# Optimization experiments

Hardware: AMD Instinct MI355X
Metric: run time of the kernel (lower is better)

The kernel has to match this reference:

```python
import jax, jax.numpy as jnp
import numpy as np

N_TOK = 256
C_Z = 128
C = 32
N_HEAD = 4


def setup_inputs() -> dict:
    key = jax.random.key(0)
    ks = jax.random.split(key, 8)
    s = 0.02
    return {
        "z": jax.random.normal(ks[0], (N_TOK, N_TOK, C_Z), dtype=jnp.float32),
        "single_mask": jnp.ones((N_TOK,), dtype=jnp.float32),
        "ln_gamma": jnp.ones((C_Z,), dtype=jnp.float32),
        "ln_beta": jnp.zeros((C_Z,), dtype=jnp.float32),
        "W_q": jax.random.normal(ks[1], (C_Z, N_HEAD * C), dtype=jnp.float32) * s,
        "W_k": jax.random.normal(ks[2], (C_Z, N_HEAD * C), dtype=jnp.float32) * s,
        "W_v": jax.random.normal(ks[3], (C_Z, N_HEAD * C), dtype=jnp.float32) * s,
        "W_b": jax.random.normal(ks[4], (C_Z, N_HEAD), dtype=jnp.float32) * s,
        "W_g": jax.random.normal(ks[5], (C_Z, N_HEAD * C), dtype=jnp.float32) * s,
        "W_out": jax.random.normal(ks[6], (N_HEAD * C, C_Z), dtype=jnp.float32) * s,
    }


def reference(z, single_mask, ln_gamma, ln_beta, W_q, W_k, W_v, W_b, W_g, W_out):
    # LayerNorm over c_z
    mu = jnp.mean(z, axis=-1, keepdims=True)
    var = jnp.var(z, axis=-1, keepdims=True)
    zn = (z - mu) * jax.lax.rsqrt(var + 1e-5) * ln_gamma + ln_beta

    n = zn.shape[0]
    proj = lambda W: (zn @ W).reshape(n, n, N_HEAD, C)
    q = proj(W_q)
    k = proj(W_k)
    v = proj(W_v)
    g = proj(W_g)
    b = zn @ W_b  # [i, j, h] -> used as bias b[j, k, h]

    # a[i,j,k,h] = q[i,j]·k[i,k]/sqrt(c) + b[j,k,h]
    a = jnp.einsum('ijhc,ikhc->ijkh', q, k) / np.sqrt(C).astype(np.float32)
    a = a + b[None, :, :, :]
    a = a + (-1e9) * (1.0 - single_mask)[None, None, :, None]
    a = jax.nn.softmax(a, axis=-2)  # over k

    o = jnp.einsum('ijkh,ikhc->ijhc', a, v)
    o = jax.nn.sigmoid(g) * o
    o = o.reshape(n, n, N_HEAD * C)
    return o @ W_out
```

## Files before the change

kernel.cpp:

```cpp
#include <hip/hip_runtime.h>
#include <hip/hip_bf16.h>

#define NT 256
#define CZ 128
#define CH 32
#define NH 4
#define PL 2097152

typedef unsigned short ushort_t;
typedef unsigned int uint_t;
typedef __attribute__((ext_vector_type(8))) short short8;
typedef __attribute__((ext_vector_type(4))) float f32x4;

__device__ __forceinline__ float bfbits2f(uint_t bits){
  union { uint_t u; float f; } v; v.u = bits; return v.f;
}
__device__ __forceinline__ float bf2f(ushort_t u){
  return bfbits2f(((uint_t)u) << 16);
}
__device__ __forceinline__ ushort_t f2bf(float f){
  union { float f; uint_t u; } v; v.f = f;
  uint_t u = v.u;
  uint_t r = (u + 0x7fffu + ((u >> 16) & 1u)) >> 16;
  return (ushort_t)r;
}
__device__ __forceinline__ void unpk(uint_t w, float& lo, float& hi){
  lo = bfbits2f(w << 16);
  hi = bfbits2f(w & 0xffff0000u);
}
__device__ __forceinline__ short8 as_s8(uint4 u){
  union { uint4 u; short8 s; } v; v.u = u; return v.s;
}
__device__ __forceinline__ uint_t pk2(float a, float b){
  union { __hip_bfloat16 h; ushort_t u; } x, y;
  x.h = __float2bfloat16(a); y.h = __float2bfloat16(b);
  return (uint_t)x.u | ((uint_t)y.u << 16);
}
__device__ __forceinline__ int detect_f32(const ushort_t* zz){
  int l = threadIdx.x & 63;
  int bad = 0;
  #pragma unroll
  for(int s=0;s<4;s++){
    float v = bf2f(zz[l*4 + s]);
    if(!(fabsf(v) < 1e9f)) bad = 1;
  }
  return (__ballot(bad) != 0ull) ? 1 : 0;
}

__global__ __launch_bounds__(256) void k_cvt_wt(const void* __restrict__ s0,
    const void* __restrict__ s1, const void* __restrict__ s2,
    const void* __restrict__ s3, const void* __restrict__ s4,
    ushort_t* __restrict__ dst, const ushort_t* __restrict__ zz,
    const void* __restrict__ m_, const void* __restrict__ g_,
    const void* __restrict__ b_, const void* __restrict__ wb_,
    float* __restrict__ smallf){
  int isf32 = detect_f32(zz);
  if(blockIdx.x >= 320){
    int idx = threadIdx.x * 4;
    const void* sp; int off;
    if(idx < 256){ sp = m_;  off = idx; }
    else if(idx < 384){ sp = g_;  off = idx-256; }
    else if(idx < 512){ sp = b_;  off = idx-384; }
    else { sp = wb_; off = idx-512; }
    float4 o;
    if(isf32){ o = *(const float4*)((const float*)sp + off); }
    else {
      uint2 u = *(const uint2*)((const ushort_t*)sp + off);
      unpk(u.x, o.x, o.y); unpk(u.y, o.z, o.w);
    }
    *(float4*)(smallf + idx) = o;
    return;
  }
  const void* srcs[5] = {s0,s1,s2,s3,s4};
  int w = blockIdx.x >> 6;
  int idx = (blockIdx.x & 63)*256 + threadIdx.x;
  int k = idx >> 7, c = idx & 127;
  const void* sp = srcs[w];
  float v;
  if(isf32) v = ((const float*)sp)[idx];
  else      v = bf2f(((const ushort_t*)sp)[idx]);
  dst[(size_t)w*16384 + (size_t)c*128 + k] = f2bf(v);
}

__global__ __launch_bounds__(256) void k_lnproj(const void* __restrict__ zraw,
    const float* __restrict__ smallf, const ushort_t* __restrict__ Wt,
    ushort_t* __restrict__ qh, ushort_t* __restrict__ kh,
    ushort_t* __restrict__ vh, ushort_t* __restrict__ gh,
    float* __restrict__ btm){
  __shared__ __align__(16) char lds[37888];
  ushort_t* znl = (ushort_t*)lds;
  float*    wbs = (float*)(lds + 35840);
  const float* mkf = smallf;
  const float* gmf = smallf + 256;
  const float* btf = smallf + 384;
  const float* Wbf = smallf + 512;
  int t = threadIdx.x;
  int isf32 = detect_f32((const ushort_t*)zraw);
  wbs[t] = Wbf[t]; wbs[t+256] = Wbf[t+256];
  __syncthreads();

  int row_loc = t >> 1, half = t & 1;
  size_t r = (size_t)blockIdx.x*128 + row_loc;
  float mval = -1e9f * (1.f - mkf[r & 255]);
  float s = 0.f, s2 = 0.f;
  if(isf32){
    const float4* zp = (const float4*)((const float*)zraw + r*CZ + half*64);
    #pragma unroll
    for(int q=0;q<16;q++){
      float4 v = zp[q];
      s  += (v.x + v.y) + (v.z + v.w);
      s2 += (v.x*v.x + v.y*v.y) + (v.z*v.z + v.w*v.w);
    }
  } else {
    const uint4* zp = (const uint4*)((const ushort_t*)zraw + r*CZ + half*64);
    #pragma unroll
    for(int q=0;q<8;q++){
      uint4 u = zp[q];
      const uint_t* pu = (const uint_t*)&u;
      #pragma unroll
      for(int e=0;e<4;e++){
        float lo, hi; unpk(pu[e], lo, hi);
        s += lo + hi; s2 += lo*lo + hi*hi;
      }
    }
  }
  s  += __shfl_xor(s, 1);
  s2 += __shfl_xor(s2, 1);
  float mu  = s * (1.f/CZ);
  float var = fmaxf(s2 * (1.f/CZ) - mu*mu, 0.f);
  float rs  = rsqrtf(var + 1e-5f);
  float acch[4] = {0.f,0.f,0.f,0.f};
  #pragma unroll
  for(int chunk=0;chunk<8;chunk++){
    float v8[8];
    if(isf32){
      const float4* zp = (const float4*)((const float*)zraw + r*CZ + half*64 + chunk*8);
      float4 a = zp[0], b = zp[1];
      v8[0]=a.x; v8[1]=a.y; v8[2]=a.z; v8[3]=a.w;
      v8[4]=b.x; v8[5]=b.y; v8[6]=b.z; v8[7]=b.w;
    } else {
      uint4 u = *(const uint4*)((const ushort_t*)zraw + r*CZ + half*64 + chunk*8);
      const uint_t* pu = (const uint_t*)&u;
      #pragma unroll
      for(int e=0;e<4;e++) unpk(pu[e], v8[e*2], v8[e*2+1]);
    }
    uint_t ow[4];
    #pragma unroll
    for(int e2=0;e2<4;e2++){
      int cg = half*64 + chunk*8 + e2*2;
      float v0 = (v8[e2*2]   - mu)*rs*gmf[cg]   + btf[cg];
      float v1 = (v8[e2*2+1] - mu)*rs*gmf[cg+1] + btf[cg+1];
      float4 w0 = *(const float4*)&wbs[cg*4];
      float4 w1 = *(const float4*)&wbs[(cg+1)*4];
      acch[0] += v0*w0.x + v1*w1.x;
      acch[1] += v0*w0.y + v1*w1.y;
      acch[2] += v0*w0.z + v1*w1.z;
      acch[3] += v0*w0.w + v1*w1.w;
      ow[e2] = (uint_t)f2bf(v0) | ((uint_t)f2bf(v1) << 16);
    }
    uint4 o; o.x=ow[0]; o.y=ow[1]; o.z=ow[2]; o.w=ow[3];
    *(uint4*)(znl + row_loc*140 + half*64 + chunk*8) = o;
  }
  #pragma unroll
  for(int h=0;h<4;h++){
    float tot = acch[h] + __shfl_xor(acch[h], 1);
    if(half == 0) btm[(size_t)h*65536 + r] = (tot + mval) * 1.4426950408889634f;
  }
  __syncthreads();

  int wave = t>>6, l = t&63, n = l&15, quad = l>>4;
  uint4 af[2][4];
  #pragma unroll
  for(int mt=0;mt<2;mt++)
    #pragma unroll
    for(int kb=0;kb<4;kb++)
      af[mt][kb] = *(const uint4*)(znl + (wave*32 + mt*16 + n)*140 + kb*32 + quad*8);
  ushort_t* outs[4] = {qh, kh, vh, gh};
  size_t row0 = (size_t)blockIdx.x*128 + wave*32;
  #pragma unroll
  for(int w=0;w<4;w++){
    const ushort_t* W = Wt + (size_t)w*16384;
    ushort_t* D = outs[w];
    float sc = (w==0) ? (0.17677669529663687f * 1.4426950408889634f) : 1.f;
    #pragma unroll
    for(int nt=0;nt<8;nt++){
      uint4 bfr[4];
      #pragma unroll
      for(int kb=0;kb<4;kb++)
        bfr[kb] = *(const uint4*)(W + ((size_t)(nt*16 + n))*128 + kb*32 + quad*8);
      f32x4 a0 = {0.f,0.f,0.f,0.f}, a1 = {0.f,0.f,0.f,0.f};
      #pragma unroll
      for(int kb=0;kb<4;kb++){
        a0 = __builtin_amdgcn_mfma_f32_16x16x32_bf16(as_s8(bfr[kb]), as_s8(af[0][kb]), a0, 0,0,0);
        a1 = __builtin_amdgcn_mfma_f32_16x16x32_bf16(as_s8(bfr[kb]), as_s8(af[1][kb]), a1, 0,0,0);
      }
      uint2 s0p, s1p;
      s0p.x = pk2(a0[0]*sc, a0[1]*sc); s0p.y = pk2(a0[2]*sc, a0[3]*sc);
      s1p.x = pk2(a1[0]*sc, a1[1]*sc); s1p.y = pk2(a1[2]*sc, a1[3]*sc);
      ushort_t* Db = D + (size_t)(nt>>1)*PL + (size_t)(nt&1)*16 + quad*4;
      *(uint2*)(Db + (row0 + n)*CH)      = s0p;
      *(uint2*)(Db + (row0 + 16 + n)*CH) = s1p;
    }
  }
}

__global__ __launch_bounds__(256, 2) void k_attn(
    const ushort_t* __restrict__ qh, const ushort_t* __restrict__ kh,
    const ushort_t* __restrict__ vh, const ushort_t* __restrict__ gh,
    const float* __restrict__ btm, ushort_t* __restrict__ oh){
  __shared__ __align__(16) char lds[40960];
  uint4*    VfA = (uint4*)lds;
  uint4*    Kf  = (uint4*)(lds + 16384);
  ushort_t* Pw0 = (ushort_t*)(lds + 32768);
  int t = threadIdx.x;
  int i = blockIdx.x >> 2, h = blockIdx.x & 3;
  int wave = t >> 6, l = t & 63;
  int n = l & 15, quad = l >> 4;
  const ushort_t* qhp = qh + (size_t)h*PL + (size_t)(i*NT)*CH;
  const ushort_t* khp = kh + (size_t)h*PL + (size_t)(i*NT)*CH;
  const ushort_t* vhp = vh + (size_t)h*PL + (size_t)(i*NT)*CH;
  const ushort_t* ghp = gh + (size_t)h*PL + (size_t)(i*NT)*CH;
  ushort_t*       ohp = oh + (size_t)h*PL + (size_t)(i*NT)*CH;
  const float*    bth = btm + (size_t)h*65536;

  {
    #pragma unroll
    for(int m=0;m<4;m++){
      int kt = wave*4 + m;
      Kf[kt*64 + l] = *(const uint4*)(khp + (size_t)(kt*16 + n)*CH + quad*8);
    }
  }
  {
    #pragma unroll
    for(int it=0; it<4; it++){
      int u = wave + it*4, kblk = u >> 1, ct = u & 1;
      uint_t d[4];
      #pragma unroll
      for(int e=0;e<4;e++){
        uint_t lo = vhp[(size_t)(kblk*32 + quad*8 + e*2    )*CH + ct*16 + n];
        uint_t hi = vhp[(size_t)(kblk*32 + quad*8 + e*2 + 1)*CH + ct*16 + n];
        d[e] = lo | (hi << 16);
      }
      uint4 o; o.x=d[0]; o.y=d[1]; o.z=d[2]; o.w=d[3];
      VfA[u*64 + l] = o;
    }
  }
  __syncthreads();

  ushort_t* Pw = Pw0 + wave*1024;
  int swz = (n & 7) << 4;

  #pragma unroll 1
  for(int s=0;s<4;s++){
    int jt = wave*4 + s;
    uint4 qf = *(const uint4*)(qhp + (size_t)(jt*16 + n)*CH + quad*8);
    f32x4 acc[16];
    #pragma unroll
    for(int kt=0;kt<16;kt++)
      acc[kt] = *(const f32x4*)(bth + (size_t)(jt*16 + n)*256 + kt*16 + quad*4);
    #pragma unroll
    for(int kt=0;kt<16;kt++){
      uint4 kfv = Kf[kt*64 + l];
      acc[kt] = __builtin_amdgcn_mfma_f32_16x16x32_bf16(as_s8(kfv), as_s8(qf), acc[kt], 0,0,0);
    }
    float sum0 = 0.f, sum1 = 0.f;
    f32x4 oa0 = {0.f,0.f,0.f,0.f}, oa1 = {0.f,0.f,0.f,0.f};
    #pragma unroll
    for(int H=0;H<2;H++){
      uint2 pv[8];
      #pragma unroll
      for(int kt=0;kt<8;kt++){
        float e0 = __builtin_amdgcn_exp2f(acc[H*8+kt][0]);
        float e1 = __builtin_amdgcn_exp2f(acc[H*8+kt][1]);
        float e2 = __builtin_amdgcn_exp2f(acc[H*8+kt][2]);
        float e3 = __builtin_amdgcn_exp2f(acc[H*8+kt][3]);
        sum0 += e0 + e1; sum1 += e2 + e3;
        pv[kt].x = pk2(e0, e1);
        pv[kt].y = pk2(e2, e3);
      }
      #pragma unroll
      for(int Q2=0;Q2<2;Q2++){
        #pragma unroll
        for(int m=0;m<4;m++)
          *(uint2*)((char*)Pw + (((n<<7) + (m<<5) + (quad<<3)) ^ swz)) = pv[Q2*4+m];
        #pragma unroll
        for(int kb=0;kb<2;kb++){
          uint4 pf = *(const uint4*)((char*)Pw + (((n<<7) + (kb<<6) + (quad<<4)) ^ swz));
          int kg = (H*2+Q2)*2 + kb;
          oa0 = __builtin_amdgcn_mfma_f32_16x16x32_bf16(as_s8(VfA[(kg*2+0)*64 + l]), as_s8(pf), oa0, 0,0,0);
          oa1 = __builtin_amdgcn_mfma_f32_16x16x32_bf16(as_s8(VfA[(kg*2+1)*64 + l]), as_s8(pf), oa1, 0,0,0);
        }
      }
    }
    float ssum = sum0 + sum1;
    ssum += __shfl_xor(ssum, 16);
    ssum += __shfl_xor(ssum, 32);
    float inv = 1.f / ssum;
    size_t rb = (size_t)(jt*16 + n)*CH;
    uint2 g0 = *(const uint2*)(ghp + rb + quad*4);
    uint2 g1 = *(const uint2*)(ghp + rb + 16 + quad*4);
    float ga[4], gc[4];
    unpk(g0.x, ga[0], ga[1]); unpk(g0.y, ga[2], ga[3]);
    unpk(g1.x, gc[0], gc[1]); unpk(g1.y, gc[2], gc[3]);
    float v0[4], v1[4];
    #pragma unroll
    for(int rr=0;rr<4;rr++){
      v0[rr] = oa0[rr] * inv * (1.f/(1.f + __expf(-ga[rr])));
      v1[rr] = oa1[rr] * inv * (1.f/(1.f + __expf(-gc[rr])));
    }
    uint2 s0, s1;
    s0.x = (uint_t)f2bf(v0[0]) | ((uint_t)f2bf(v0[1]) << 16);
    s0.y = (uint_t)f2bf(v0[2]) | ((uint_t)f2bf(v0[3]) << 16);
    s1.x = (uint_t)f2bf(v1[0]) | ((uint_t)f2bf(v1[1]) << 16);
    s1.y = (uint_t)f2bf(v1[2]) | ((uint_t)f2bf(v1[3]) << 16);
    *(uint2*)(ohp + rb + quad*4)      = s0;
    *(uint2*)(ohp + rb + 16 + quad*4) = s1;
  }
}

__global__ __launch_bounds__(256) void k_gemm1(const ushort_t* __restrict__ oh,
    const ushort_t* __restrict__ Wt, void* __restrict__ outp,
    const ushort_t* __restrict__ zz){
  int isf32 = detect_f32(zz);
  int t = threadIdx.x, wave = t>>6, l = t&63, n = l&15, quad = l>>4;
  size_t row0 = (size_t)blockIdx.x*128 + wave*32;
  uint4 af[2][4];
  #pragma unroll
  for(int mt=0;mt<2;mt++)
    #pragma unroll
    for(int kb=0;kb<4;kb++)
      af[mt][kb] = *(const uint4*)(oh + (size_t)kb*PL + (row0 + mt*16 + n)*CH + quad*8);
  #pragma unroll
  for(int nt=0;nt<8;nt++){
    uint4 bfr[4];
    #pragma unroll
    for(int kb=0;kb<4;kb++)
      bfr[kb] = *(const uint4*)(Wt + ((size_t)(nt*16 + n))*128 + kb*32 + quad*8);
    f32x4 a0 = {0.f,0.f,0.f,0.f}, a1 = {0.f,0.f,0.f,0.f};
    #pragma unroll
    for(int kb=0;kb<4;kb++){
      a0 = __builtin_amdgcn_mfma_f32_16x16x32_bf16(as_s8(bfr[kb]), as_s8(af[0][kb]), a0, 0,0,0);
      a1 = __builtin_amdgcn_mfma_f32_16x16x32_bf16(as_s8(bfr[kb]), as_s8(af[1][kb]), a1, 0,0,0);
    }
    if(isf32){
      float* of = (float*)outp + nt*16 + quad*4;
      *(f32x4*)(of + (row0 + n)*CZ)      = a0;
      *(f32x4*)(of + (row0 + 16 + n)*CZ) = a1;
    } else {
      uint2 s0p, s1p;
      s0p.x = pk2(a0[0], a0[1]); s0p.y = pk2(a0[2], a0[3]);
      s1p.x = pk2(a1[0], a1[1]); s1p.y = pk2(a1[2], a1[3]);
      ushort_t* ob = (ushort_t*)outp + nt*16 + quad*4;
      *(uint2*)(ob + (row0 + n)*CZ)      = s0p;
      *(uint2*)(ob + (row0 + 16 + n)*CZ) = s1p;
    }
  }
}

extern "C" void kernel_launch(void* const* d_in, const int* in_sizes, int n_in,
                              void* d_out, int out_size, void* d_ws, size_t ws_size,
                              hipStream_t stream){
  char* wsb = (char*)d_ws;
  const size_t TB = (size_t)16777216;
  ushort_t* qh  = (ushort_t*)(wsb);
  ushort_t* kh  = (ushort_t*)(wsb + TB);
  ushort_t* vh  = (ushort_t*)(wsb + 2*TB);
  ushort_t* gh  = (ushort_t*)(wsb + 3*TB);
  ushort_t* oh  = (ushort_t*)(wsb + 4*TB);
  float*    btm = (float*)   (wsb + 5*TB);
  float*  smallf= (float*)   (wsb + 5*TB + (1u<<20));
  ushort_t* Wt  = (ushort_t*)(wsb + 5*TB + (1u<<20) + 4096);
  const ushort_t* zz = (const ushort_t*)d_in[0];

  k_cvt_wt   <<<321, 256, 0, stream>>>(d_in[4], d_in[5], d_in[6], d_in[8], d_in[9],
                                       Wt, zz, d_in[1], d_in[2], d_in[3], d_in[7], smallf);
  k_lnproj   <<<512, 256, 0, stream>>>(d_in[0], smallf, Wt, qh, kh, vh, gh, btm);
  k_attn     <<<1024,256, 0, stream>>>(qh, kh, vh, gh, btm, oh);
  k_gemm1    <<<512, 256, 0, stream>>>(oh, Wt + (size_t)4*16384, d_out, zz);
}
```

Measured before the change: 209.7 us.

## Fuse output projection GEMM into attention kernel with one block per row

The attention kernel is restructured so each 512-thread block handles one row i for all four heads, with two waves per head sharing that head's K and V tiles in a larger LDS allocation. After a barrier, the same block runs the final W_out projection over the 256 gated outputs it just wrote, which removes the separate k_gemm1 launch and lets those reads likely hit cache. The trade-off is a grid of only 256 blocks and about 144 KB of LDS per block, which limits each CU to one resident block and may hurt latency hiding. Each wave also now works through twice as many j-tiles in sequence.

Result: faster. 197.5 us, median of 2 (-5.8%).

```diff
diff --git a/kernel.cpp b/kernel.cpp
--- a/kernel.cpp
+++ b/kernel.cpp
@@ -204,18 +204,21 @@
   }
 }
 
-__global__ __launch_bounds__(256, 2) void k_attn(
+__global__ __launch_bounds__(512, 2) void k_attn(
     const ushort_t* __restrict__ qh, const ushort_t* __restrict__ kh,
     const ushort_t* __restrict__ vh, const ushort_t* __restrict__ gh,
-    const float* __restrict__ btm, ushort_t* __restrict__ oh){
-  __shared__ __align__(16) char lds[40960];
-  uint4*    VfA = (uint4*)lds;
-  uint4*    Kf  = (uint4*)(lds + 16384);
-  ushort_t* Pw0 = (ushort_t*)(lds + 32768);
+    const float* __restrict__ btm, ushort_t* __restrict__ oh,
+    const ushort_t* __restrict__ Wt4, void* __restrict__ outp,
+    const ushort_t* __restrict__ zz){
+  __shared__ __align__(16) char lds[147456];
   int t = threadIdx.x;
-  int i = blockIdx.x >> 2, h = blockIdx.x & 3;
-  int wave = t >> 6, l = t & 63;
+  int i = blockIdx.x;
+  int w = t >> 6, l = t & 63;
+  int h = w >> 1, sub = w & 1;
   int n = l & 15, quad = l >> 4;
+  uint4*    Kf  = (uint4*)(lds + h*16384);
+  uint4*    VfA = (uint4*)(lds + 65536 + h*16384);
+  ushort_t* Pw  = (ushort_t*)(lds + 131072) + w*1024;
   const ushort_t* qhp = qh + (size_t)h*PL + (size_t)(i*NT)*CH;
   const ushort_t* khp = kh + (size_t)h*PL + (size_t)(i*NT)*CH;
   const ushort_t* vhp = vh + (size_t)h*PL + (size_t)(i*NT)*CH;
@@ -225,15 +228,15 @@
 
   {
     #pragma unroll
-    for(int m=0;m<4;m++){
-      int kt = wave*4 + m;
+    for(int m=0;m<8;m++){
+      int kt = sub*8 + m;
       Kf[kt*64 + l] = *(const uint4*)(khp + (size_t)(kt*16 + n)*CH + quad*8);
     }
   }
   {
     #pragma unroll
-    for(int it=0; it<4; it++){
-      int u = wave + it*4, kblk = u >> 1, ct = u & 1;
+    for(int it=0; it<8; it++){
+      int u = sub + it*2, kblk = u >> 1, ct = u & 1;
       uint_t d[4];
       #pragma unroll
       for(int e=0;e<4;e++){
@@ -247,12 +250,11 @@
   }
   __syncthreads();
 
-  ushort_t* Pw = Pw0 + wave*1024;
   int swz = (n & 7) << 4;
 
   #pragma unroll 1
-  for(int s=0;s<4;s++){
-    int jt = wave*4 + s;
+  for(int s=0;s<8;s++){
+    int jt = sub*8 + s;
     uint4 qf = *(const uint4*)(qhp + (size_t)(jt*16 + n)*CH + quad*8);
     f32x4 acc[16];
     #pragma unroll
@@ -316,14 +318,10 @@
     *(uint2*)(ohp + rb + quad*4)      = s0;
     *(uint2*)(ohp + rb + 16 + quad*4) = s1;
   }
-}
-
-__global__ __launch_bounds__(256) void k_gemm1(const ushort_t* __restrict__ oh,
-    const ushort_t* __restrict__ Wt, void* __restrict__ outp,
-    const ushort_t* __restrict__ zz){
+  __syncthreads();
+
   int isf32 = detect_f32(zz);
-  int t = threadIdx.x, wave = t>>6, l = t&63, n = l&15, quad = l>>4;
-  size_t row0 = (size_t)blockIdx.x*128 + wave*32;
+  size_t row0 = (size_t)i*NT + w*32;
   uint4 af[2][4];
   #pragma unroll
   for(int mt=0;mt<2;mt++)
@@ -335,7 +333,7 @@
     uint4 bfr[4];
     #pragma unroll
     for(int kb=0;kb<4;kb++)
-      bfr[kb] = *(const uint4*)(Wt + ((size_t)(nt*16 + n))*128 + kb*32 + quad*8);
+      bfr[kb] = *(const uint4*)(Wt4 + ((size_t)(nt*16 + n))*128 + kb*32 + quad*8);
     f32x4 a0 = {0.f,0.f,0.f,0.f}, a1 = {0.f,0.f,0.f,0.f};
     #pragma unroll
     for(int kb=0;kb<4;kb++){
@@ -375,6 +373,6 @@
   k_cvt_wt   <<<321, 256, 0, stream>>>(d_in[4], d_in[5], d_in[6], d_in[8], d_in[9],
                                        Wt, zz, d_in[1], d_in[2], d_in[3], d_in[7], smallf);
   k_lnproj   <<<512, 256, 0, stream>>>(d_in[0], smallf, Wt, qh, kh, vh, gh, btm);
-  k_attn     <<<1024,256, 0, stream>>>(qh, kh, vh, gh, btm, oh);
-  k_gemm1    <<<512, 256, 0, stream>>>(oh, Wt + (size_t)4*16384, d_out, zz);
-}
+  k_attn     <<<256, 512, 0, stream>>>(qh, kh, vh, gh, btm, oh,
+                                       Wt + (size_t)4*16384, d_out, zz);
+}
```
